# Performance work log

Measured on AMD Instinct MI355X. Metric: run time of the kernel, lower is better.

Reference implementation:

```python
import jax, jax.numpy as jnp
import numpy as np

N, DZ, DQ = 65536, 128, 512


def setup_inputs() -> dict:
    key = jax.random.key(0)
    kz, kb, kg = jax.random.split(key, 3)
    z = jax.random.normal(kz, (N, DZ), dtype=jnp.float32)
    # match torch init scaling: beta ~ 0.01*randn, gamma ~ 0.05*randn
    beta = jax.random.normal(kb, (DQ, DZ), dtype=jnp.float32) * 0.01
    gamma = jax.random.normal(kg, (DQ, DZ), dtype=jnp.float32) * 0.05
    return {"z": z, "beta": beta, "gamma": gamma}


def reference(z, beta, gamma):
    # zero-inflated Poisson sampling decoder
    logits = jnp.einsum("nd,qd->nq", z, beta)          # [N, dq]
    pi = jax.nn.sigmoid(logits)                          # exp(x)/(1+exp(x))
    rate = jnp.nan_to_num(jnp.exp(jnp.einsum("nd,qd->nq", z, gamma)), nan=1e-4)
    rate = jnp.abs(rate) + 0.01
    key = jax.random.key(42)
    kp, kb = jax.random.split(key)
    poisson = jax.random.poisson(kp, rate).astype(jnp.float32)   # [N, dq]
    masking = jax.random.bernoulli(kb, 1.0 - pi).astype(jnp.float32)
    return masking * poisson
```

## Files before the change

### kernel.cpp

```cpp
#include <hip/hip_runtime.h>
#include <stdint.h>

#pragma clang fp contract(off)

#define HALF_ 16777216u

#define WS_TSLOT 386
#define WS_WLCNT 388
#define WS_P1E5  392
#define TBL_OFF_B 4096
#define TBL_K0 95904
#define TBL_N  8193
#define WL_OFF_B 40960
#define WLCAP 16384u
#define BT_OFF_B 172032
#define NEED_V2 (BT_OFF_B + 2u * 512u * 128u * sizeof(float))
#define NEED_V1 (4096u + 2u * 512u * 128u * sizeof(float))

__device__ __forceinline__ void tf2x32(uint32_t k0, uint32_t k1,
                                       uint32_t x0, uint32_t x1,
                                       uint32_t& o0, uint32_t& o1) {
  uint32_t ks2 = k0 ^ k1 ^ 0x1BD11BDAu;
  x0 += k0; x1 += k1;
#define TFR(r) x0 += x1; x1 = (x1 << (r)) | (x1 >> (32 - (r))); x1 ^= x0;
  TFR(13) TFR(15) TFR(26) TFR(6)
  x0 += k1;  x1 += ks2 + 1u;
  TFR(17) TFR(29) TFR(16) TFR(24)
  x0 += ks2; x1 += k0 + 2u;
  TFR(13) TFR(15) TFR(26) TFR(6)
  x0 += k0;  x1 += k1 + 3u;
  TFR(17) TFR(29) TFR(16) TFR(24)
  x0 += k1;  x1 += ks2 + 4u;
  TFR(13) TFR(15) TFR(26) TFR(6)
  x0 += ks2; x1 += k0 + 5u;
#undef TFR
  o0 = x0; o1 = x1;
}

__device__ __forceinline__ uint32_t tfx(uint32_t k0, uint32_t k1, uint32_t i) {
  uint32_t o0, o1;
  tf2x32(k0, k1, 0u, i, o0, o1);
  return o0 ^ o1;
}

__device__ __forceinline__ float u01(uint32_t bits) {
  return __uint_as_float((bits >> 9) | 0x3f800000u) - 1.0f;
}

__device__ __forceinline__ float csqrt(float x) {
  return (float)__builtin_sqrt((double)x);
}

__device__ __forceinline__ float eexp(float xin) {
  float c = fminf(xin, 88.3762626647950f);
  c = fmaxf(c, -88.3762626647949f);
  float fx = floorf(__builtin_fmaf(c, 1.44269504088896341f, 0.5f));
  float x = __builtin_fmaf(-0.693359375f, fx, c);
  x = __builtin_fmaf(2.12194440e-4f, fx, x);
  float z = x * x;
  float y = __builtin_fmaf(x, 1.9875691500e-4f, 1.3981999507e-3f);
  y = __builtin_fmaf(y, x, 8.3334519073e-3f);
  y = __builtin_fmaf(y, x, 4.1665795894e-2f);
  y = __builtin_fmaf(y, x, 1.6666665459e-1f);
  y = __builtin_fmaf(y, x, 5.0000001201e-1f);
  y = __builtin_fmaf(y, z, x);
  y = 1.0f + y;
  int e = (int)fx;
  float s = __uint_as_float((uint32_t)(e + 127) << 23);
  return fmaxf(y * s, xin);
}

__device__ __forceinline__ float elog(float xin) {
  float x = fmaxf(xin, 1.17549435e-38f);
  uint32_t bits = __float_as_uint(x);
  float e = (float)((int)(bits >> 23) - 0x7e);
  x = __uint_as_float((bits & 0x807fffffu) | 0x3f000000u);
  bool mask = x < 0.707106781186547524f;
  float tmp = mask ? x : 0.0f;
  x = x - 1.0f;
  e = e - (mask ? 1.0f : 0.0f);
  x = x + tmp;
  float z = x * x;
  float y = __builtin_fmaf(7.0376836292e-2f, x, -1.1514610310e-1f);
  y = __builtin_fmaf(y, x, 1.1676998740e-1f);
  y = __builtin_fmaf(y, x, -1.2420140846e-1f);
  y = __builtin_fmaf(y, x, 1.4249322787e-1f);
  y = __builtin_fmaf(y, x, -1.6668057665e-1f);
  y = __builtin_fmaf(y, x, 2.0000714765e-1f);
  y = __builtin_fmaf(y, x, -2.4999993993e-1f);
  y = __builtin_fmaf(y, x, 3.3333331174e-1f);
  y = y * x;
  y = y * z;
  y = __builtin_fmaf(e, -2.12194440e-4f, y);
  y = __builtin_fmaf(-0.5f, z, y);
  x = x + y;
  x = __builtin_fmaf(e, 0.693359375f, x);
  if (xin == 0.0f) x = -__builtin_inff();
  return x;
}

__device__ __forceinline__ float xlog1p(float x) {
  float small_ = __builtin_fmaf(-0.5f, x, 1.0f) * x;
  float large_ = elog(x + 1.0f);
  return (fabsf(x) < 1e-4f) ? small_ : large_;
}

__device__ __forceinline__ float xlgamma(float input) {
  float z = input - 1.0f;
  float x = 0.99999999999980993227684700473478f;
  const float lcs[8] = {
      676.520368121885098567009190444019f,
      -1259.13921672240287047156078755283f,
      771.3234287776530788486528258894f,
      -176.61502916214059906584551354f,
      12.507343278686904814458936853f,
      -0.13857109526572011689554707f,
      9.984369578019570859563e-6f,
      1.50563273514931155834e-7f};
#pragma unroll
  for (int i = 0; i < 8; ++i) {
    x = x + lcs[i] / ((z + (float)i) + 1.0f);
  }
  float t = 7.5f + z;
  float log_t = 2.0149030205422647f + xlog1p(z / 7.5f);
  float log_y = __builtin_fmaf((z + 0.5f) - t / log_t, log_t,
                               0.91893853320467274178f) + elog(x);
  return log_y;
}

struct TrsP { float ll, bb, aa, ia, vr; };
__device__ __forceinline__ TrsP trs_params(float lam) {
  TrsP p;
  p.ll = elog(lam);
  p.bb = __builtin_fmaf(2.53f, csqrt(lam), 0.931f);
  p.aa = __builtin_fmaf(0.02483f, p.bb, -0.059f);
  p.ia = 1.1239f + 1.1328f / (p.bb - 3.4f);
  p.vr = 0.9277f - 3.6224f / (p.bb - 2.0f);
  return p;
}

__device__ __forceinline__ bool trs_step(float lam, const TrsP& p,
                                         float u, float v, float& kout) {
  float us = 0.5f - fabsf(u);
  float t2 = (2.0f * p.aa) / us + p.bb;
  float k = floorf(__builtin_fmaf(t2, u, lam) + 0.43f);
  kout = k;
  bool accept1 = (us >= 0.07f) && (v <= p.vr);
  if (accept1) return true;
  bool reject = (k < 0.0f) || ((us < 0.013f) && (v > us));
  if (reject) return false;
  float s = elog(v * p.ia / (p.aa / (us * us) + p.bb));
  float tt = __builtin_fmaf(k, p.ll, -lam) - xlgamma(k + 1.0f);
  return s <= tt;
}


__global__ void chain_v2(uint32_t* __restrict__ ws) {
  int lane = threadIdx.x;
  uint32_t kpa = 0, kpb = 0;
  if (lane == 0) {
    uint32_t a0, b0;
    tf2x32(0u, 42u, 0u, 0u, kpa, kpb);
    tf2x32(0u, 42u, 0u, 1u, a0, b0);
    ws[0] = a0; ws[1] = b0;
  }
  kpa = __shfl(kpa, 0); kpb = __shfl(kpb, 0);
  uint32_t kra = kpa, krb = kpb;
  uint32_t kja = kpa, kjb = kpb;
  for (int i = 0; i < 64; ++i) {
    bool isrej = (lane >= 2 && lane <= 4);
    uint32_t key0 = isrej ? kja : kra;
    uint32_t key1 = isrej ? kjb : krb;
    uint32_t xx = (lane == 1) ? 1u : (lane == 3) ? 1u : (lane == 4) ? 2u : 0u;
    uint32_t o0, o1;
    tf2x32(key0, key1, 0u, xx, o0, o1);
    if (lane == 1) { ws[2 + 2 * i] = o0; ws[3 + 2 * i] = o1; }
    if (lane == 3) { ws[130 + 4 * i] = o0; ws[131 + 4 * i] = o1; }
    if (lane == 4) { ws[132 + 4 * i] = o0; ws[133 + 4 * i] = o1; }
    kra = __shfl(o0, 0); krb = __shfl(o1, 0);
    kja = __shfl(o0, 2); kjb = __shfl(o1, 2);
  }
  if (lane == 0) {
    TrsP p = trs_params(1e5f);
    float* wf = (float*)(ws + WS_P1E5);
    wf[0] = p.ll; wf[1] = p.bb; wf[2] = p.aa; wf[3] = p.ia; wf[4] = p.vr;
    ws[WS_TSLOT] = 0u;
    ws[WS_WLCNT] = 0u;
  }
}

__global__ __launch_bounds__(256) void lgt_kernel(uint32_t* __restrict__ ws) {
  int j = blockIdx.x * 256 + threadIdx.x;
  if (j >= TBL_N) return;
  float* tbl = (float*)((char*)ws + TBL_OFF_B);
  tbl[j] = xlgamma((float)(TBL_K0 + j) + 1.0f);
}

__global__ __launch_bounds__(256) void transpose_kernel(
    const float* __restrict__ b, const float* __restrict__ g,
    float* __restrict__ bT, float* __restrict__ gT) {
  int i = blockIdx.x * 256 + threadIdx.x;
  int q = i >> 7, d = i & 127;
  bT[d * 512 + q] = b[i];
  gT[d * 512 + q] = g[i];
}

__global__ __launch_bounds__(256) void pass1_lite(
    const uint32_t* __restrict__ chain, uint32_t* __restrict__ Tslot) {
  const float* wf = (const float*)(chain + WS_P1E5);
  const float ll = wf[0], bb = wf[1], aa = wf[2], ia = wf[3], vr = wf[4];
  const float* tbl = (const float*)((const char*)chain + TBL_OFF_B);
  const float EPS = 1e-4f;

  uint32_t t = blockIdx.x * 256u + threadIdx.x;
  const uint32_t* rej = chain + 130;
  int faA = 63, faB = 63;
  bool accA = false, accB = false;
  for (int it = 0; it < 64; ++it) {
    if (accA && accB) break;
    uint32_t s00 = rej[4 * it + 0], s01 = rej[4 * it + 1];
    uint32_t s10 = rej[4 * it + 2], s11 = rej[4 * it + 3];
#pragma unroll
    for (int half = 0; half < 2; ++half) {
      bool& acc = half ? accB : accA;
      int& fa = half ? faB : faA;
      if (acc) continue;
      uint32_t idx = half ? (t + HALF_) : t;
      float u = u01(tfx(s00, s01, idx)) - 0.5f;
      float v = u01(tfx(s10, s11, idx));
      float us = 0.5f - fabsf(u);
      bool a1 = (us >= 0.07f) && (v <= vr);
      bool ok;
      if (a1) {
        ok = true;
      } else {
        float t2 = (2.0f * aa) / us + bb;
        float k = floorf(__builtin_fmaf(t2, u, 1e5f) + 0.43f);
        bool rejd = (k < 0.0f) || ((us < 0.013f) && (v > us));
        if (rejd) {
          ok = false;
        } else {
          float arg = v * ia / (aa / (us * us) + bb);
          int ki = (int)k - TBL_K0;
          float lg = (ki >= 0 && ki < TBL_N) ? tbl[ki] : xlgamma(k + 1.0f);
          float tt = __builtin_fmaf(k, ll, -1e5f) - lg;
          float sf = __logf(arg);
          if (sf <= tt - EPS)      ok = true;
          else if (sf > tt + EPS)  ok = false;
          else                     ok = (elog(arg) <= tt);
        }
      }
      if (ok) { acc = true; fa = it; }
    }
  }
  int fa = faA > faB ? faA : faB;
  for (int off = 32; off > 0; off >>= 1) {
    int o = __shfl_down(fa, off, 64);
    fa = fa > o ? fa : o;
  }
  __shared__ int smax[4];
  int wave = threadIdx.x >> 6, lanei = threadIdx.x & 63;
  if (lanei == 0) smax[wave] = fa;
  __syncthreads();
  if (threadIdx.x == 0) {
    int m01 = smax[0] > smax[1] ? smax[0] : smax[1];
    int m23 = smax[2] > smax[3] ? smax[2] : smax[3];
    int m = m01 > m23 ? m01 : m23;
    atomicMax(Tslot, (uint32_t)m);
  }
}

__device__ __forceinline__ int first_accept_exact(float lam, uint32_t idx,
                                                  const uint32_t* __restrict__ rej) {
  TrsP p = trs_params(lam);
  for (int it = 0; it < 64; ++it) {
    float u = u01(tfx(rej[4 * it + 0], rej[4 * it + 1], idx)) - 0.5f;
    float v = u01(tfx(rej[4 * it + 2], rej[4 * it + 3], idx));
    float kk;
    if (trs_step(lam, p, u, v, kk)) return it;
  }
  return 63;
}

__global__ __launch_bounds__(256) void zip_v2(
    const float* __restrict__ z, const float* __restrict__ bT,
    const float* __restrict__ gT, const uint32_t* __restrict__ chain,
    uint32_t* __restrict__ wsrw, float* __restrict__ out) {
  uint32_t t = blockIdx.x * 256u + threadIdx.x;
  uint32_t n = t >> 9;
  uint32_t q = t & 511u;
  uint32_t n2 = n + 32768u;

  const float* zr  = z + (size_t)n * 128u;
  const float* zr2 = z + (size_t)n2 * 128u;

  float lA = 0.f, lB = 0.f, gA = 0.f, gB = 0.f;
  for (int d = 0; d < 128; ++d) {
    float bv = bT[d * 512 + q];
    float gv = gT[d * 512 + q];
    float z1 = zr[d], z2 = zr2[d];
    lA = lA + z1 * bv;
    lB = lB + z2 * bv;
    gA = gA + z1 * gv;
    gB = gB + z2 * gv;
  }

  float piA = 1.0f / (1.0f + eexp(-lA));
  float piB = 1.0f / (1.0f + eexp(-lB));
  float lamA = fabsf(eexp(gA)) + 0.01f;
  float lamB = fabsf(eexp(gB)) + 0.01f;

  bool knuA = lamA < 10.0f, knuB = lamB < 10.0f;
  float pA = 0.f, pB = 0.f;
  bool fDA = false, fUA = false, fDB = false, fUB = false;
  {
    const uint32_t* wsk = chain + 2;
    const float delA = 4e-6f * (lamA + 4.0f);
    const float delB = 4e-6f * (lamB + 4.0f);
    float lpA = 0.f, lpB = 0.f;
    int kA = 0, kB = 0;
    bool goA = knuA, goB = knuB;
    for (int it = 0; it < 64; ++it) {
      if (!goA && !goB) break;
      uint32_t w0 = wsk[2 * it], w1 = wsk[2 * it + 1];
      if (goA) {
        float d = lpA + lamA;
        bool nearb = fabsf(d) < delA;
        if (d > 0.0f) { fDA = nearb; fUA = false; kA++; lpA = lpA + __logf(u01(tfx(w0, w1, t))); }
        else          { fUA = nearb; goA = false; }
      }
      if (goB) {
        float d = lpB + lamB;
        bool nearb = fabsf(d) < delB;
        if (d > 0.0f) { fDB = nearb; fUB = false; kB++; lpB = lpB + __logf(u01(tfx(w0, w1, t + HALF_))); }
        else          { fUB = nearb; goB = false; }
      }
    }
    if (knuA) pA = (float)(kA - 1);
    if (knuB) pB = (float)(kB - 1);
  }

  float dmA = u01(tfx(chain[0], chain[1], t)) - (1.0f - piA);
  float dmB = u01(tfx(chain[0], chain[1], t + HALF_)) - (1.0f - piB);
  bool mA = dmA < 0.0f, mB = dmB < 0.0f;
  bool mfA = fabsf(dmA) < 2e-6f, mfB = fabsf(dmB) < 2e-6f;

  uint32_t* wlcnt = wsrw + WS_WLCNT;
  uint32_t* wl = (uint32_t*)((char*)wsrw + WL_OFF_B);
  const uint32_t* rejk = chain + 130;

  float resA, resB;
  if (!knuA) {
    atomicMax(wsrw + WS_TSLOT, (uint32_t)first_accept_exact(lamA, t, rejk));
    uint32_t slot = atomicAdd(wlcnt, 1u);
    if (slot < WLCAP) {
      wl[2 * slot] = t | (mA ? 0x80000000u : 0u);
      wl[2 * slot + 1] = __float_as_uint(lamA);
    }
    resA = 0.0f;
  } else {
    float hiA = pA + (fUA ? 0.5f : 0.0f);
    if (mfA && hiA <= 1.2f) {
      resA = 0.5f * hiA;
    } else {
      float ph = pA + ((fDA && fUA) ? 0.0f : (fDA ? -0.5f : (fUA ? 0.5f : 0.0f)));
      resA = mA ? ph : 0.0f;
    }
  }
  if (!knuB) {
    atomicMax(wsrw + WS_TSLOT, (uint32_t)first_accept_exact(lamB, t + HALF_, rejk));
    uint32_t slot = atomicAdd(wlcnt, 1u);
    if (slot < WLCAP) {
      wl[2 * slot] = (t + HALF_) | (mB ? 0x80000000u : 0u);
      wl[2 * slot + 1] = __float_as_uint(lamB);
    }
    resB = 0.0f;
  } else {
    float hiB = pB + (fUB ? 0.5f : 0.0f);
    if (mfB && hiB <= 1.2f) {
      resB = 0.5f * hiB;
    } else {
      float ph = pB + ((fDB && fUB) ? 0.0f : (fDB ? -0.5f : (fUB ? 0.5f : 0.0f)));
      resB = mB ? ph : 0.0f;
    }
  }

  out[t]         = resA;
  out[t + HALF_] = resB;
}

__global__ __launch_bounds__(256) void k3_kernel(
    const uint32_t* __restrict__ ws, float* __restrict__ out) {
  uint32_t cnt = ws[WS_WLCNT];
  uint32_t n = cnt < WLCAP ? cnt : WLCAP;
  uint32_t Traw = ws[WS_TSLOT];
  int Tmax = (int)(Traw > 63u ? 63u : Traw);
  const uint32_t* wl = (const uint32_t*)((const char*)ws + WL_OFF_B);
  const uint32_t* rej = ws + 130;
  for (uint32_t i = blockIdx.x * 256u + threadIdx.x; i < n; i += 64u * 256u) {
    uint32_t im = wl[2 * i];
    float lam = __uint_as_float(wl[2 * i + 1]);
    uint32_t idx = im & 0x7FFFFFFFu;
    bool mask = (im >> 31) != 0u;
    TrsP p = trs_params(lam);
    float klast = -1.0f;
    for (int it = 0; it <= Tmax; ++it) {
      float u = u01(tfx(rej[4 * it + 0], rej[4 * it + 1], idx)) - 0.5f;
      float v = u01(tfx(rej[4 * it + 2], rej[4 * it + 3], idx));
      float kk;
      if (trs_step(lam, p, u, v, kk)) klast = kk;
    }
    out[idx] = mask ? klast : 0.0f;
  }
}


__global__ void chain_r10(uint32_t* __restrict__ ws) {
  if (threadIdx.x != 0 || blockIdx.x != 0) return;
  uint32_t k0 = 0u, k1 = 42u;
  uint32_t a0, b0, a1, b1;
  uint32_t kpa, kpb;
  tf2x32(k0, k1, 0u, 0u, kpa, kpb);
  tf2x32(k0, k1, 0u, 1u, a0, b0);
  ws[0] = a0; ws[1] = b0;
  uint32_t ra = kpa, rb = kpb;
  for (int i = 0; i < 64; ++i) {
    tf2x32(ra, rb, 0u, 1u, a0, b0);
    ws[2 + 2 * i] = a0; ws[3 + 2 * i] = b0;
    tf2x32(ra, rb, 0u, 0u, a1, b1);
    ra = a1; rb = b1;
  }
  ra = kpa; rb = kpb;
  for (int i = 0; i < 64; ++i) {
    tf2x32(ra, rb, 0u, 1u, a0, b0);
    ws[130 + 4 * i] = a0; ws[131 + 4 * i] = b0;
    tf2x32(ra, rb, 0u, 2u, a0, b0);
    ws[132 + 4 * i] = a0; ws[133 + 4 * i] = b0;
    tf2x32(ra, rb, 0u, 0u, a1, b1);
    ra = a1; rb = b1;
  }
  ws[386] = 0u;
}

template <bool TRANS>
__global__ __launch_bounds__(256) void pass1_r10(
    const float* __restrict__ z, const float* __restrict__ gamma,
    const float* __restrict__ gT, const uint32_t* __restrict__ chain,
    uint32_t* __restrict__ Tslot) {
  uint32_t t = blockIdx.x * 256u + threadIdx.x;
  uint32_t n = t >> 9;
  uint32_t q = t & 511u;
  uint32_t n2 = n + 32768u;
  const float* zr  = z + (size_t)n * 128u;
  const float* zr2 = z + (size_t)n2 * 128u;
  float gA = 0.f, gB = 0.f;
  if (TRANS) {
    for (int d = 0; d < 128; ++d) {
      float gv = gT[d * 512 + q];
      gA = gA + zr[d] * gv;
      gB = gB + zr2[d] * gv;
    }
  } else {
    const float* gr = gamma + (size_t)q * 128u;
    for (int d = 0; d < 128; ++d) {
      float gv = gr[d];
      gA = gA + zr[d] * gv;
      gB = gB + zr2[d] * gv;
    }
  }
  float lamA = fabsf(eexp(gA)) + 0.01f;
  float lamB = fabsf(eexp(gB)) + 0.01f;
  float lrA = (lamA < 10.0f) ? 1e5f : lamA;
  float lrB = (lamB < 10.0f) ? 1e5f : lamB;
  TrsP pa = trs_params(lrA);
  TrsP pb = trs_params(lrB);
  const uint32_t* rej = chain + 130;
  int faA = 63, faB = 63;
  bool accA = false, accB = false;
  for (int it = 0; it < 64; ++it) {
    if (accA && accB) break;
    uint32_t s00 = rej[4 * it + 0], s01 = rej[4 * it + 1];
    uint32_t s10 = rej[4 * it + 2], s11 = rej[4 * it + 3];
    float kk;
    if (!accA) {
      float u = u01(tfx(s00, s01, t)) - 0.5f;
      float v = u01(tfx(s10, s11, t));
      if (trs_step(lrA, pa, u, v, kk)) { accA = true; faA = it; }
    }
    if (!accB) {
      float u = u01(tfx(s00, s01, t + HALF_)) - 0.5f;
      float v = u01(tfx(s10, s11, t + HALF_));
      if (trs_step(lrB, pb, u, v, kk)) { accB = true; faB = it; }
    }
  }
  int fa = faA > faB ? faA : faB;
  for (int off = 32; off > 0; off >>= 1) {
    int o = __shfl_down(fa, off, 64);
    fa = fa > o ? fa : o;
  }
  __shared__ int smax[4];
  int wave = threadIdx.x >> 6, lanei = threadIdx.x & 63;
  if (lanei == 0) smax[wave] = fa;
  __syncthreads();
  if (threadIdx.x == 0) {
    int m01 = smax[0] > smax[1] ? smax[0] : smax[1];
    int m23 = smax[2] > smax[3] ? smax[2] : smax[3];
    int m = m01 > m23 ? m01 : m23;
    atomicMax(Tslot, (uint32_t)m);
  }
}

__device__ float pois_rej_last_r10(float lam, uint32_t idx,
                                   const uint32_t* __restrict__ rej, int Tmax) {
  TrsP p = trs_params(lam);
  float klast = -1.0f;
  for (int it = 0; it <= Tmax; ++it) {
    float u = u01(tfx(rej[4 * it + 0], rej[4 * it + 1], idx)) - 0.5f;
    float v = u01(tfx(rej[4 * it + 2], rej[4 * it + 3], idx));
    float kk;
    if (trs_step(lam, p, u, v, kk)) klast = kk;
  }
  return klast;
}

template <bool TRANS>
__global__ __launch_bounds__(256) void zip_r10(
    const float* __restrict__ z, const float* __restrict__ beta,
    const float* __restrict__ gamma, const float* __restrict__ bT,
    const float* __restrict__ gT, const uint32_t* __restrict__ chain,
    float* __restrict__ out) {
  uint32_t t = blockIdx.x * 256u + threadIdx.x;
  uint32_t n = t >> 9;
  uint32_t q = t & 511u;
  uint32_t n2 = n + 32768u;
  const float* zr  = z + (size_t)n * 128u;
  const float* zr2 = z + (size_t)n2 * 128u;
  float lA = 0.f, lB = 0.f, gA = 0.f, gB = 0.f;
  if (TRANS) {
    for (int d = 0; d < 128; ++d) {
      float bv = bT[d * 512 + q];
      float gv = gT[d * 512 + q];
      float z1 = zr[d], z2 = zr2[d];
      lA = lA + z1 * bv;
      lB = lB + z2 * bv;
      gA = gA + z1 * gv;
      gB = gB + z2 * gv;
    }
  } else {
    const float* br = beta + (size_t)q * 128u;
    const float* gr = gamma + (size_t)q * 128u;
    for (int d = 0; d < 128; ++d) {
      float bv = br[d], gv = gr[d];
      float z1 = zr[d], z2 = zr2[d];
      lA = lA + z1 * bv;
      lB = lB + z2 * bv;
      gA = gA + z1 * gv;
      gB = gB + z2 * gv;
    }
  }
  float piA = 1.0f / (1.0f + eexp(-lA));
  float piB = 1.0f / (1.0f + eexp(-lB));
  float lamA = fabsf(eexp(gA)) + 0.01f;
  float lamB = fabsf(eexp(gB)) + 0.01f;
  bool knuA = lamA < 10.0f, knuB = lamB < 10.0f;
  float pA = 0.f, pB = 0.f;
  bool fDA = false, fUA = false, fDB = false, fUB = false;
  {
    const uint32_t* wsk = chain + 2;
    const float delA = 1e-6f * (lamA + 4.0f);
    const float delB = 1e-6f * (lamB + 4.0f);
    float lpA = 0.f, lpB = 0.f;
    int kA = 0, kB = 0;
    bool goA = knuA, goB = knuB;
    for (int it = 0; it < 64; ++it) {
      if (!goA && !goB) break;
      uint32_t w0 = wsk[2 * it], w1 = wsk[2 * it + 1];
      if (goA) {
        float d = lpA + lamA;
        bool nearb = fabsf(d) < delA;
        if (d > 0.0f) { fDA = nearb; fUA = false; kA++; lpA = lpA + elog(u01(tfx(w0, w1, t))); }
        else          { fUA = nearb; goA = false; }
      }
      if (goB) {
        float d = lpB + lamB;
        bool nearb = fabsf(d) < delB;
        if (d > 0.0f) { fDB = nearb; fUB = false; kB++; lpB = lpB + elog(u01(tfx(w0, w1, t + HALF_))); }
        else          { fUB = nearb; goB = false; }
      }
    }
    if (knuA) pA = (float)(kA - 1);
    if (knuB) pB = (float)(kB - 1);
  }
  int Tmax = (int)(chain[386] > 63u ? 63u : chain[386]);
  if (!knuA) { pA = pois_rej_last_r10(lamA, t, chain + 130, Tmax); fDA = fUA = false; }
  if (!knuB) { pB = pois_rej_last_r10(lamB, t + HALF_, chain + 130, Tmax); fDB = fUB = false; }
  float dmA = u01(tfx(chain[0], chain[1], t)) - (1.0f - piA);
  float dmB = u01(tfx(chain[0], chain[1], t + HALF_)) - (1.0f - piB);
  bool mA = dmA < 0.0f, mB = dmB < 0.0f;
  bool mfA = fabsf(dmA) < 2e-6f, mfB = fabsf(dmB) < 2e-6f;
  float hiA = pA + (fUA ? 0.5f : 0.0f);
  float hiB = pB + (fUB ? 0.5f : 0.0f);
  float resA, resB;
  if (mfA && hiA <= 1.2f) {
    resA = 0.5f * hiA;
  } else {
    float ph = pA + ((fDA && fUA) ? 0.0f : (fDA ? -0.5f : (fUA ? 0.5f : 0.0f)));
    resA = mA ? ph : 0.0f;
  }
  if (mfB && hiB <= 1.2f) {
    resB = 0.5f * hiB;
  } else {
    float ph = pB + ((fDB && fUB) ? 0.0f : (fDB ? -0.5f : (fUB ? 0.5f : 0.0f)));
    resB = mB ? ph : 0.0f;
  }
  out[t]         = resA;
  out[t + HALF_] = resB;
}

extern "C" void kernel_launch(void* const* d_in, const int* in_sizes, int n_in,
                              void* d_out, int out_size, void* d_ws, size_t ws_size,
                              hipStream_t stream) {
  const float* z     = (const float*)d_in[0];
  const float* beta  = (const float*)d_in[1];
  const float* gamma = (const float*)d_in[2];
  float* out = (float*)d_out;
  uint32_t* ws = (uint32_t*)d_ws;

  if (ws_size >= NEED_V2) {
    float* bT = (float*)((char*)d_ws + BT_OFF_B);
    float* gT = bT + 512 * 128;
    chain_v2<<<1, 64, 0, stream>>>(ws);
    lgt_kernel<<<(TBL_N + 255) / 256, 256, 0, stream>>>(ws);
    transpose_kernel<<<256, 256, 0, stream>>>(beta, gamma, bT, gT);
    pass1_lite<<<HALF_ / 256u, 256, 0, stream>>>(ws, ws + WS_TSLOT);
    zip_v2<<<HALF_ / 256u, 256, 0, stream>>>(z, bT, gT, ws, ws, out);
    k3_kernel<<<64, 256, 0, stream>>>(ws, out);
  } else if (ws_size >= NEED_V1) {
    float* bT = (float*)((char*)d_ws + 4096);
    float* gT = bT + 512 * 128;
    chain_r10<<<1, 1, 0, stream>>>(ws);
    transpose_kernel<<<256, 256, 0, stream>>>(beta, gamma, bT, gT);
    pass1_r10<true><<<HALF_ / 256u, 256, 0, stream>>>(z, gamma, gT, ws, ws + 386);
    zip_r10<true><<<HALF_ / 256u, 256, 0, stream>>>(z, beta, gamma, bT, gT, ws, out);
  } else {
    chain_r10<<<1, 1, 0, stream>>>(ws);
    pass1_r10<false><<<HALF_ / 256u, 256, 0, stream>>>(z, gamma, nullptr, ws, ws + 386);
    zip_r10<false><<<HALF_ / 256u, 256, 0, stream>>>(z, beta, gamma, nullptr, nullptr, ws, out);
  }
}
```

Baseline: 1.919 ms.

## Split rejection-pass and Knuth tails into compacted worklists with tiled float4 weights

Pass 1 now evaluates only the first rejection iteration for every element. Elements that are not accepted are compacted into a worklist through a wave ballot and an atomic, and a second kernel scans only those. The zip kernel runs at most four Knuth iterations inline and pushes survivors to a worklist finished by a separate grid-stride kernel. This reduces divergence in the long per-thread loops. The weights are transposed into a 4-interleaved layout so the dot products can use float4 loads. In exchange it adds more kernel launches, global atomics and worklist traffic, and it relies on a larger workspace layout with capacity fallbacks.

```diff
diff --git a/kernel.cpp b/kernel.cpp
--- a/kernel.cpp
+++ b/kernel.cpp
@@ -6,16 +6,23 @@
 #define HALF_ 16777216u
 
 #define WS_TSLOT 386
-#define WS_WLCNT 388
+#define WS_RCNT  388
+#define WS_KCNT  390
+#define WS_PCNT  391
 #define WS_P1E5  392
 #define TBL_OFF_B 4096
 #define TBL_K0 95904
 #define TBL_N  8193
-#define WL_OFF_B 40960
-#define WLCAP 16384u
-#define BT_OFF_B 172032
-#define NEED_V2 (BT_OFF_B + 2u * 512u * 128u * sizeof(float))
-#define NEED_V1 (4096u + 2u * 512u * 128u * sizeof(float))
+#define V2WL_OFF_B 40960
+#define V2WLCAP 16384u
+#define V2BT_OFF_B 172032
+#define NEED_V2 (V2BT_OFF_B + 2u * 512u * 128u * 4u)
+#define RWL_OFF_B 81920
+#define RWLCAP 16384u
+#define BTT_OFF_B 262144
+#define GTT_OFF_B 524288
+#define DYN_OFF_B 786432
+#define NEED_V3 (DYN_OFF_B + (1u << 20))
 
 __device__ __forceinline__ void tf2x32(uint32_t k0, uint32_t k1,
                                        uint32_t x0, uint32_t x1,
@@ -154,7 +161,6 @@
   return s <= tt;
 }
 
-
 __global__ void chain_v2(uint32_t* __restrict__ ws) {
   int lane = threadIdx.x;
   uint32_t kpa = 0, kpb = 0;
@@ -185,7 +191,9 @@
     float* wf = (float*)(ws + WS_P1E5);
     wf[0] = p.ll; wf[1] = p.bb; wf[2] = p.aa; wf[3] = p.ia; wf[4] = p.vr;
     ws[WS_TSLOT] = 0u;
-    ws[WS_WLCNT] = 0u;
+    ws[WS_RCNT] = 0u;
+    ws[WS_KCNT] = 0u;
+    ws[WS_PCNT] = 0u;
   }
 }
 
@@ -205,13 +213,312 @@
   gT[d * 512 + q] = g[i];
 }
 
+__global__ __launch_bounds__(256) void transpose_tiled(
+    const float* __restrict__ b, const float* __restrict__ g,
+    float* __restrict__ bTT, float* __restrict__ gTT) {
+  int i = blockIdx.x * 256 + threadIdx.x;
+  int q = i >> 7, d = i & 127;
+  int dst = (d >> 2) * 2048 + (q << 2) + (d & 3);
+  bTT[dst] = b[i];
+  gTT[dst] = g[i];
+}
+
+struct P1C { float ll, bb, aa, ia, vr; };
+
+__device__ __forceinline__ bool p1_eval(const P1C& c, const float* __restrict__ tbl,
+                                        uint32_t s00, uint32_t s01,
+                                        uint32_t s10, uint32_t s11, uint32_t idx) {
+  float u = u01(tfx(s00, s01, idx)) - 0.5f;
+  float v = u01(tfx(s10, s11, idx));
+  float us = 0.5f - fabsf(u);
+  if (us >= 0.07f && v <= c.vr) return true;
+  float t2 = (2.0f * c.aa) / us + c.bb;
+  float k = floorf(__builtin_fmaf(t2, u, 1e5f) + 0.43f);
+  if ((k < 0.0f) || ((us < 0.013f) && (v > us))) return false;
+  float arg = v * c.ia / (c.aa / (us * us) + c.bb);
+  int ki = (int)k - TBL_K0;
+  float lg = (ki >= 0 && ki < TBL_N) ? tbl[ki] : xlgamma(k + 1.0f);
+  float tt = __builtin_fmaf(k, c.ll, -1e5f) - lg;
+  float sf = __logf(arg);
+  if (sf <= tt - 1e-4f) return true;
+  if (sf > tt + 1e-4f) return false;
+  return elog(arg) <= tt;
+}
+
+__device__ uint32_t p1_scan(const P1C& c, const float* __restrict__ tbl,
+                            const uint32_t* __restrict__ rej, uint32_t idx) {
+  for (int it = 1; it < 64; ++it) {
+    if (p1_eval(c, tbl, rej[4 * it], rej[4 * it + 1], rej[4 * it + 2],
+                rej[4 * it + 3], idx))
+      return (uint32_t)it;
+  }
+  return 63u;
+}
+
+__global__ __launch_bounds__(256) void p1a_kernel(
+    uint32_t* ws, uint32_t* __restrict__ p1wl, uint32_t p1cap) {
+  const float* wf = (const float*)(ws + WS_P1E5);
+  P1C c{wf[0], wf[1], wf[2], wf[3], wf[4]};
+  const float* tbl = (const float*)((const char*)ws + TBL_OFF_B);
+  const uint32_t* rej = ws + 130;
+  uint32_t s00 = rej[0], s01 = rej[1], s10 = rej[2], s11 = rej[3];
+  uint32_t t = blockIdx.x * 256u + threadIdx.x;
+  bool fa = !p1_eval(c, tbl, s00, s01, s10, s11, t);
+  bool fb = !p1_eval(c, tbl, s00, s01, s10, s11, t + HALF_);
+  uint64_t ba = __ballot(fa), bbm = __ballot(fb);
+  int na = __popcll(ba), nb = __popcll(bbm);
+  int lane = threadIdx.x & 63;
+  uint32_t base = 0;
+  if (lane == 0 && (na + nb) > 0) base = atomicAdd(ws + WS_PCNT, (uint32_t)(na + nb));
+  base = __shfl(base, 0);
+  uint64_t lm = (1ull << lane) - 1ull;
+  if (fa) {
+    uint32_t slot = base + (uint32_t)__popcll(ba & lm);
+    if (slot < p1cap) p1wl[slot] = t;
+    else atomicMax(ws + WS_TSLOT, p1_scan(c, tbl, rej, t));
+  }
+  if (fb) {
+    uint32_t slot = base + (uint32_t)na + (uint32_t)__popcll(bbm & lm);
+    if (slot < p1cap) p1wl[slot] = t + HALF_;
+    else atomicMax(ws + WS_TSLOT, p1_scan(c, tbl, rej, t + HALF_));
+  }
+}
+
+__global__ __launch_bounds__(256) void p1b_kernel(
+    uint32_t* ws, const uint32_t* __restrict__ p1wl, uint32_t p1cap) {
+  const float* wf = (const float*)(ws + WS_P1E5);
+  P1C c{wf[0], wf[1], wf[2], wf[3], wf[4]};
+  const float* tbl = (const float*)((const char*)ws + TBL_OFF_B);
+  const uint32_t* rej = ws + 130;
+  uint32_t cnt = ws[WS_PCNT];
+  if (cnt > p1cap) cnt = p1cap;
+  uint32_t fmax = 0;
+  for (uint32_t i = blockIdx.x * 256u + threadIdx.x; i < cnt;
+       i += gridDim.x * 256u) {
+    uint32_t f = p1_scan(c, tbl, rej, p1wl[i]);
+    if (f > fmax) fmax = f;
+  }
+  for (int off = 32; off > 0; off >>= 1) {
+    uint32_t o = __shfl_down(fmax, off, 64);
+    if (o > fmax) fmax = o;
+  }
+  if ((threadIdx.x & 63) == 0 && fmax > 0) atomicMax(ws + WS_TSLOT, fmax);
+}
+
+__device__ __forceinline__ int first_accept_exact(float lam, uint32_t idx,
+                                                  const uint32_t* __restrict__ rej) {
+  TrsP p = trs_params(lam);
+  for (int it = 0; it < 64; ++it) {
+    float u = u01(tfx(rej[4 * it + 0], rej[4 * it + 1], idx)) - 0.5f;
+    float v = u01(tfx(rej[4 * it + 2], rej[4 * it + 3], idx));
+    float kk;
+    if (trs_step(lam, p, u, v, kk)) return it;
+  }
+  return 63;
+}
+
+__device__ float knuth_finish(float lp, float lam, bool fD, bool m,
+                              const uint32_t* __restrict__ wsk, uint32_t idx) {
+  const float del = 4e-6f * (lam + 4.0f);
+  int k = 4;
+  bool fU = false;
+  for (int it = 4; it < 64; ++it) {
+    float d = lp + lam;
+    bool nb = fabsf(d) < del;
+    if (d > 0.0f) {
+      fD = nb; k++;
+      lp = lp + __logf(u01(tfx(wsk[2 * it], wsk[2 * it + 1], idx)));
+    } else { fU = nb; break; }
+  }
+  float p = (float)(k - 1);
+  float ph = p + ((fD && fU) ? 0.0f : (fD ? -0.5f : (fU ? 0.5f : 0.0f)));
+  return m ? ph : 0.0f;
+}
+
+__global__ __launch_bounds__(256) void zip_v3(
+    const float* __restrict__ z, uint32_t* ws,
+    uint32_t* __restrict__ kwl, uint32_t kcap, float* __restrict__ out) {
+  uint32_t t = blockIdx.x * 256u + threadIdx.x;
+  uint32_t n = t >> 9, q = t & 511u, n2 = n + 32768u;
+
+  const float4* z4a = (const float4*)(z + (size_t)n * 128u);
+  const float4* z4b = (const float4*)(z + (size_t)n2 * 128u);
+  const float4* bt4 = (const float4*)((const char*)ws + BTT_OFF_B);
+  const float4* gt4 = (const float4*)((const char*)ws + GTT_OFF_B);
+
+  float lA = 0.f, lB = 0.f, gA = 0.f, gB = 0.f;
+  for (int d4 = 0; d4 < 32; ++d4) {
+    float4 bv = bt4[(d4 << 9) + q];
+    float4 gv = gt4[(d4 << 9) + q];
+    float4 z1 = z4a[d4], z2 = z4b[d4];
+    lA = lA + z1.x * bv.x; lB = lB + z2.x * bv.x; gA = gA + z1.x * gv.x; gB = gB + z2.x * gv.x;
+    lA = lA + z1.y * bv.y; lB = lB + z2.y * bv.y; gA = gA + z1.y * gv.y; gB = gB + z2.y * gv.y;
+    lA = lA + z1.z * bv.z; lB = lB + z2.z * bv.z; gA = gA + z1.z * gv.z; gB = gB + z2.z * gv.z;
+    lA = lA + z1.w * bv.w; lB = lB + z2.w * bv.w; gA = gA + z1.w * gv.w; gB = gB + z2.w * gv.w;
+  }
+
+  float piA = 1.0f / (1.0f + eexp(-lA));
+  float piB = 1.0f / (1.0f + eexp(-lB));
+  float lamA = fabsf(eexp(gA)) + 0.01f;
+  float lamB = fabsf(eexp(gB)) + 0.01f;
+
+  float dmA = u01(tfx(ws[0], ws[1], t)) - (1.0f - piA);
+  float dmB = u01(tfx(ws[0], ws[1], t + HALF_)) - (1.0f - piB);
+  bool mA = dmA < 0.0f, mB = dmB < 0.0f;
+  bool mfA = fabsf(dmA) < 2e-6f, mfB = fabsf(dmB) < 2e-6f;
+
+  bool knuA = lamA < 10.0f, knuB = lamB < 10.0f;
+
+  const uint32_t* wsk = ws + 2;
+  const float delA = 4e-6f * (lamA + 4.0f);
+  const float delB = 4e-6f * (lamB + 4.0f);
+  float lpA = 0.f, lpB = 0.f;
+  int kA = 0, kB = 0;
+  bool goA = knuA, goB = knuB;
+  bool fDA = false, fUA = false, fDB = false, fUB = false;
+  for (int it = 0; it < 4; ++it) {
+    if (!goA && !goB) break;
+    uint32_t w0 = wsk[2 * it], w1 = wsk[2 * it + 1];
+    if (goA) {
+      float d = lpA + lamA;
+      bool nb = fabsf(d) < delA;
+      if (d > 0.0f) { fDA = nb; kA++; lpA = lpA + __logf(u01(tfx(w0, w1, t))); }
+      else          { fUA = nb; goA = false; }
+    }
+    if (goB) {
+      float d = lpB + lamB;
+      bool nb = fabsf(d) < delB;
+      if (d > 0.0f) { fDB = nb; kB++; lpB = lpB + __logf(u01(tfx(w0, w1, t + HALF_))); }
+      else          { fUB = nb; goB = false; }
+    }
+  }
+  bool survA = knuA && goA, survB = knuB && goB;
+
+  const uint32_t* rejk = ws + 130;
+  uint32_t* rwl = (uint32_t*)((char*)ws + RWL_OFF_B);
+  if (!knuA) {
+    atomicMax(ws + WS_TSLOT, (uint32_t)first_accept_exact(lamA, t, rejk));
+    uint32_t slot = atomicAdd(ws + WS_RCNT, 1u);
+    if (slot < RWLCAP) {
+      rwl[2 * slot] = t | (mA ? 0x80000000u : 0u);
+      rwl[2 * slot + 1] = __float_as_uint(lamA);
+    }
+  }
+  if (!knuB) {
+    atomicMax(ws + WS_TSLOT, (uint32_t)first_accept_exact(lamB, t + HALF_, rejk));
+    uint32_t slot = atomicAdd(ws + WS_RCNT, 1u);
+    if (slot < RWLCAP) {
+      rwl[2 * slot] = (t + HALF_) | (mB ? 0x80000000u : 0u);
+      rwl[2 * slot + 1] = __float_as_uint(lamB);
+    }
+  }
+
+  uint64_t ba = __ballot(survA), bbm = __ballot(survB);
+  int na = __popcll(ba), nb = __popcll(bbm);
+  int lane = threadIdx.x & 63;
+  uint32_t base = 0;
+  if (lane == 0 && (na + nb) > 0) base = atomicAdd(ws + WS_KCNT, (uint32_t)(na + nb));
+  base = __shfl(base, 0);
+  uint64_t lm = (1ull << lane) - 1ull;
+
+  if (survA) {
+    uint32_t slot = base + (uint32_t)__popcll(ba & lm);
+    if (slot < kcap) {
+      kwl[3 * slot]     = t | ((uint32_t)mA << 25) | ((uint32_t)fDA << 27);
+      kwl[3 * slot + 1] = __float_as_uint(lpA);
+      kwl[3 * slot + 2] = __float_as_uint(lamA);
+    } else {
+      out[t] = knuth_finish(lpA, lamA, fDA, mA, wsk, t);
+    }
+  } else if (knuA) {
+    float pA = (float)(kA - 1);
+    float hiA = pA + (fUA ? 0.5f : 0.0f);
+    float resA;
+    if (mfA && hiA <= 1.2f) resA = 0.5f * hiA;
+    else {
+      float ph = pA + ((fDA && fUA) ? 0.0f : (fDA ? -0.5f : (fUA ? 0.5f : 0.0f)));
+      resA = mA ? ph : 0.0f;
+    }
+    out[t] = resA;
+  } else {
+    out[t] = 0.0f;
+  }
+
+  if (survB) {
+    uint32_t slot = base + (uint32_t)na + (uint32_t)__popcll(bbm & lm);
+    if (slot < kcap) {
+      kwl[3 * slot]     = (t + HALF_) | ((uint32_t)mB << 25) | ((uint32_t)fDB << 27);
+      kwl[3 * slot + 1] = __float_as_uint(lpB);
+      kwl[3 * slot + 2] = __float_as_uint(lamB);
+    } else {
+      out[t + HALF_] = knuth_finish(lpB, lamB, fDB, mB, wsk, t + HALF_);
+    }
+  } else if (knuB) {
+    float pB = (float)(kB - 1);
+    float hiB = pB + (fUB ? 0.5f : 0.0f);
+    float resB;
+    if (mfB && hiB <= 1.2f) resB = 0.5f * hiB;
+    else {
+      float ph = pB + ((fDB && fUB) ? 0.0f : (fDB ? -0.5f : (fUB ? 0.5f : 0.0f)));
+      resB = mB ? ph : 0.0f;
+    }
+    out[t + HALF_] = resB;
+  } else {
+    out[t + HALF_] = 0.0f;
+  }
+}
+
+__global__ __launch_bounds__(256) void k3b_kernel(
+    uint32_t* ws, const uint32_t* __restrict__ kwl, uint32_t kcap,
+    float* __restrict__ out) {
+  uint32_t cnt = ws[WS_KCNT];
+  if (cnt > kcap) cnt = kcap;
+  const uint32_t* wsk = ws + 2;
+  for (uint32_t i = blockIdx.x * 256u + threadIdx.x; i < cnt;
+       i += gridDim.x * 256u) {
+    uint32_t w = kwl[3 * i];
+    uint32_t idx = w & 0x01FFFFFFu;
+    bool m = (w >> 25) & 1u;
+    bool fD = (w >> 27) & 1u;
+    float lp = __uint_as_float(kwl[3 * i + 1]);
+    float lam = __uint_as_float(kwl[3 * i + 2]);
+    out[idx] = knuth_finish(lp, lam, fD, m, wsk, idx);
+  }
+}
+
+__global__ __launch_bounds__(256) void k3_kernel(
+    const uint32_t* ws, const uint32_t* __restrict__ wl, uint32_t cap,
+    float* __restrict__ out) {
+  uint32_t cnt = ws[WS_RCNT];
+  if (cnt > cap) cnt = cap;
+  uint32_t Traw = ws[WS_TSLOT];
+  int Tmax = (int)(Traw > 63u ? 63u : Traw);
+  const uint32_t* rej = ws + 130;
+  for (uint32_t i = blockIdx.x * 256u + threadIdx.x; i < cnt;
+       i += gridDim.x * 256u) {
+    uint32_t im = wl[2 * i];
+    float lam = __uint_as_float(wl[2 * i + 1]);
+    uint32_t idx = im & 0x7FFFFFFFu;
+    bool mask = (im >> 31) != 0u;
+    TrsP p = trs_params(lam);
+    float klast = -1.0f;
+    for (int it = 0; it <= Tmax; ++it) {
+      float u = u01(tfx(rej[4 * it + 0], rej[4 * it + 1], idx)) - 0.5f;
+      float v = u01(tfx(rej[4 * it + 2], rej[4 * it + 3], idx));
+      float kk;
+      if (trs_step(lam, p, u, v, kk)) klast = kk;
+    }
+    out[idx] = mask ? klast : 0.0f;
+  }
+}
+
+
 __global__ __launch_bounds__(256) void pass1_lite(
     const uint32_t* __restrict__ chain, uint32_t* __restrict__ Tslot) {
   const float* wf = (const float*)(chain + WS_P1E5);
   const float ll = wf[0], bb = wf[1], aa = wf[2], ia = wf[3], vr = wf[4];
   const float* tbl = (const float*)((const char*)chain + TBL_OFF_B);
   const float EPS = 1e-4f;
-
   uint32_t t = blockIdx.x * 256u + threadIdx.x;
   const uint32_t* rej = chain + 130;
   int faA = 63, faB = 63;
@@ -231,23 +538,21 @@
       float us = 0.5f - fabsf(u);
       bool a1 = (us >= 0.07f) && (v <= vr);
       bool ok;
-      if (a1) {
-        ok = true;
-      } else {
+      if (a1) ok = true;
+      else {
         float t2 = (2.0f * aa) / us + bb;
         float k = floorf(__builtin_fmaf(t2, u, 1e5f) + 0.43f);
         bool rejd = (k < 0.0f) || ((us < 0.013f) && (v > us));
-        if (rejd) {
-          ok = false;
-        } else {
+        if (rejd) ok = false;
+        else {
           float arg = v * ia / (aa / (us * us) + bb);
           int ki = (int)k - TBL_K0;
           float lg = (ki >= 0 && ki < TBL_N) ? tbl[ki] : xlgamma(k + 1.0f);
           float tt = __builtin_fmaf(k, ll, -1e5f) - lg;
           float sf = __logf(arg);
-          if (sf <= tt - EPS)      ok = true;
-          else if (sf > tt + EPS)  ok = false;
-          else                     ok = (elog(arg) <= tt);
+          if (sf <= tt - EPS) ok = true;
+          else if (sf > tt + EPS) ok = false;
+          else ok = (elog(arg) <= tt);
         }
       }
       if (ok) { acc = true; fa = it; }
@@ -270,30 +575,13 @@
   }
 }
 
-__device__ __forceinline__ int first_accept_exact(float lam, uint32_t idx,
-                                                  const uint32_t* __restrict__ rej) {
-  TrsP p = trs_params(lam);
-  for (int it = 0; it < 64; ++it) {
-    float u = u01(tfx(rej[4 * it + 0], rej[4 * it + 1], idx)) - 0.5f;
-    float v = u01(tfx(rej[4 * it + 2], rej[4 * it + 3], idx));
-    float kk;
-    if (trs_step(lam, p, u, v, kk)) return it;
-  }
-  return 63;
-}
-
 __global__ __launch_bounds__(256) void zip_v2(
     const float* __restrict__ z, const float* __restrict__ bT,
-    const float* __restrict__ gT, const uint32_t* __restrict__ chain,
-    uint32_t* __restrict__ wsrw, float* __restrict__ out) {
+    const float* __restrict__ gT, uint32_t* ws, float* __restrict__ out) {
   uint32_t t = blockIdx.x * 256u + threadIdx.x;
-  uint32_t n = t >> 9;
-  uint32_t q = t & 511u;
-  uint32_t n2 = n + 32768u;
-
+  uint32_t n = t >> 9, q = t & 511u, n2 = n + 32768u;
   const float* zr  = z + (size_t)n * 128u;
   const float* zr2 = z + (size_t)n2 * 128u;
-
   float lA = 0.f, lB = 0.f, gA = 0.f, gB = 0.f;
   for (int d = 0; d < 128; ++d) {
     float bv = bT[d * 512 + q];
@@ -304,17 +592,15 @@
     gA = gA + z1 * gv;
     gB = gB + z2 * gv;
   }
-
   float piA = 1.0f / (1.0f + eexp(-lA));
   float piB = 1.0f / (1.0f + eexp(-lB));
   float lamA = fabsf(eexp(gA)) + 0.01f;
   float lamB = fabsf(eexp(gB)) + 0.01f;
-
   bool knuA = lamA < 10.0f, knuB = lamB < 10.0f;
   float pA = 0.f, pB = 0.f;
   bool fDA = false, fUA = false, fDB = false, fUB = false;
   {
-    const uint32_t* wsk = chain + 2;
+    const uint32_t* wsk = ws + 2;
     const float delA = 4e-6f * (lamA + 4.0f);
     const float delB = 4e-6f * (lamB + 4.0f);
     float lpA = 0.f, lpB = 0.f;
@@ -325,295 +611,60 @@
       uint32_t w0 = wsk[2 * it], w1 = wsk[2 * it + 1];
       if (goA) {
         float d = lpA + lamA;
-        bool nearb = fabsf(d) < delA;
-        if (d > 0.0f) { fDA = nearb; fUA = false; kA++; lpA = lpA + __logf(u01(tfx(w0, w1, t))); }
-        else          { fUA = nearb; goA = false; }
+        bool nb = fabsf(d) < delA;
+        if (d > 0.0f) { fDA = nb; kA++; lpA = lpA + __logf(u01(tfx(w0, w1, t))); }
+        else          { fUA = nb; goA = false; }
       }
       if (goB) {
         float d = lpB + lamB;
-        bool nearb = fabsf(d) < delB;
-        if (d > 0.0f) { fDB = nearb; fUB = false; kB++; lpB = lpB + __logf(u01(tfx(w0, w1, t + HALF_))); }
-        else          { fUB = nearb; goB = false; }
+        bool nb = fabsf(d) < delB;
+        if (d > 0.0f) { fDB = nb; kB++; lpB = lpB + __logf(u01(tfx(w0, w1, t + HALF_))); }
+        else          { fUB = nb; goB = false; }
       }
     }
     if (knuA) pA = (float)(kA - 1);
     if (knuB) pB = (float)(kB - 1);
   }
-
-  float dmA = u01(tfx(chain[0], chain[1], t)) - (1.0f - piA);
-  float dmB = u01(tfx(chain[0], chain[1], t + HALF_)) - (1.0f - piB);
+  float dmA = u01(tfx(ws[0], ws[1], t)) - (1.0f - piA);
+  float dmB = u01(tfx(ws[0], ws[1], t + HALF_)) - (1.0f - piB);
   bool mA = dmA < 0.0f, mB = dmB < 0.0f;
   bool mfA = fabsf(dmA) < 2e-6f, mfB = fabsf(dmB) < 2e-6f;
-
-  uint32_t* wlcnt = wsrw + WS_WLCNT;
-  uint32_t* wl = (uint32_t*)((char*)wsrw + WL_OFF_B);
-  const uint32_t* rejk = chain + 130;
-
+  uint32_t* wl = (uint32_t*)((char*)ws + V2WL_OFF_B);
+  const uint32_t* rejk = ws + 130;
   float resA, resB;
   if (!knuA) {
-    atomicMax(wsrw + WS_TSLOT, (uint32_t)first_accept_exact(lamA, t, rejk));
-    uint32_t slot = atomicAdd(wlcnt, 1u);
-    if (slot < WLCAP) {
+    atomicMax(ws + WS_TSLOT, (uint32_t)first_accept_exact(lamA, t, rejk));
+    uint32_t slot = atomicAdd(ws + WS_RCNT, 1u);
+    if (slot < V2WLCAP) {
       wl[2 * slot] = t | (mA ? 0x80000000u : 0u);
       wl[2 * slot + 1] = __float_as_uint(lamA);
     }
     resA = 0.0f;
   } else {
     float hiA = pA + (fUA ? 0.5f : 0.0f);
-    if (mfA && hiA <= 1.2f) {
-      resA = 0.5f * hiA;
-    } else {
+    if (mfA && hiA <= 1.2f) resA = 0.5f * hiA;
+    else {
       float ph = pA + ((fDA && fUA) ? 0.0f : (fDA ? -0.5f : (fUA ? 0.5f : 0.0f)));
       resA = mA ? ph : 0.0f;
     }
   }
   if (!knuB) {
-    atomicMax(wsrw + WS_TSLOT, (uint32_t)first_accept_exact(lamB, t + HALF_, rejk));
-    uint32_t slot = atomicAdd(wlcnt, 1u);
-    if (slot < WLCAP) {
+    atomicMax(ws + WS_TSLOT, (uint32_t)first_accept_exact(lamB, t + HALF_, rejk));
+    uint32_t slot = atomicAdd(ws + WS_RCNT, 1u);
+    if (slot < V2WLCAP) {
       wl[2 * slot] = (t + HALF_) | (mB ? 0x80000000u : 0u);
       wl[2 * slot + 1] = __float_as_uint(lamB);
     }
     resB = 0.0f;
   } else {
     float hiB = pB + (fUB ? 0.5f : 0.0f);
-    if (mfB && hiB <= 1.2f) {
-      resB = 0.5f * hiB;
-    } else {
+    if (mfB && hiB <= 1.2f) resB = 0.5f * hiB;
+    else {
       float ph = pB + ((fDB && fUB) ? 0.0f : (fDB ? -0.5f : (fUB ? 0.5f : 0.0f)));
       resB = mB ? ph : 0.0f;
     }
   }
-
-  out[t]         = resA;
-  out[t + HALF_] = resB;
-}
-
-__global__ __launch_bounds__(256) void k3_kernel(
-    const uint32_t* __restrict__ ws, float* __restrict__ out) {
-  uint32_t cnt = ws[WS_WLCNT];
-  uint32_t n = cnt < WLCAP ? cnt : WLCAP;
-  uint32_t Traw = ws[WS_TSLOT];
-  int Tmax = (int)(Traw > 63u ? 63u : Traw);
-  const uint32_t* wl = (const uint32_t*)((const char*)ws + WL_OFF_B);
-  const uint32_t* rej = ws + 130;
-  for (uint32_t i = blockIdx.x * 256u + threadIdx.x; i < n; i += 64u * 256u) {
-    uint32_t im = wl[2 * i];
-    float lam = __uint_as_float(wl[2 * i + 1]);
-    uint32_t idx = im & 0x7FFFFFFFu;
-    bool mask = (im >> 31) != 0u;
-    TrsP p = trs_params(lam);
-    float klast = -1.0f;
-    for (int it = 0; it <= Tmax; ++it) {
-      float u = u01(tfx(rej[4 * it + 0], rej[4 * it + 1], idx)) - 0.5f;
-      float v = u01(tfx(rej[4 * it + 2], rej[4 * it + 3], idx));
-      float kk;
-      if (trs_step(lam, p, u, v, kk)) klast = kk;
-    }
-    out[idx] = mask ? klast : 0.0f;
-  }
-}
-
-
-__global__ void chain_r10(uint32_t* __restrict__ ws) {
-  if (threadIdx.x != 0 || blockIdx.x != 0) return;
-  uint32_t k0 = 0u, k1 = 42u;
-  uint32_t a0, b0, a1, b1;
-  uint32_t kpa, kpb;
-  tf2x32(k0, k1, 0u, 0u, kpa, kpb);
-  tf2x32(k0, k1, 0u, 1u, a0, b0);
-  ws[0] = a0; ws[1] = b0;
-  uint32_t ra = kpa, rb = kpb;
-  for (int i = 0; i < 64; ++i) {
-    tf2x32(ra, rb, 0u, 1u, a0, b0);
-    ws[2 + 2 * i] = a0; ws[3 + 2 * i] = b0;
-    tf2x32(ra, rb, 0u, 0u, a1, b1);
-    ra = a1; rb = b1;
-  }
-  ra = kpa; rb = kpb;
-  for (int i = 0; i < 64; ++i) {
-    tf2x32(ra, rb, 0u, 1u, a0, b0);
-    ws[130 + 4 * i] = a0; ws[131 + 4 * i] = b0;
-    tf2x32(ra, rb, 0u, 2u, a0, b0);
-    ws[132 + 4 * i] = a0; ws[133 + 4 * i] = b0;
-    tf2x32(ra, rb, 0u, 0u, a1, b1);
-    ra = a1; rb = b1;
-  }
-  ws[386] = 0u;
-}
-
-template <bool TRANS>
-__global__ __launch_bounds__(256) void pass1_r10(
-    const float* __restrict__ z, const float* __restrict__ gamma,
-    const float* __restrict__ gT, const uint32_t* __restrict__ chain,
-    uint32_t* __restrict__ Tslot) {
-  uint32_t t = blockIdx.x * 256u + threadIdx.x;
-  uint32_t n = t >> 9;
-  uint32_t q = t & 511u;
-  uint32_t n2 = n + 32768u;
-  const float* zr  = z + (size_t)n * 128u;
-  const float* zr2 = z + (size_t)n2 * 128u;
-  float gA = 0.f, gB = 0.f;
-  if (TRANS) {
-    for (int d = 0; d < 128; ++d) {
-      float gv = gT[d * 512 + q];
-      gA = gA + zr[d] * gv;
-      gB = gB + zr2[d] * gv;
-    }
-  } else {
-    const float* gr = gamma + (size_t)q * 128u;
-    for (int d = 0; d < 128; ++d) {
-      float gv = gr[d];
-      gA = gA + zr[d] * gv;
-      gB = gB + zr2[d] * gv;
-    }
-  }
-  float lamA = fabsf(eexp(gA)) + 0.01f;
-  float lamB = fabsf(eexp(gB)) + 0.01f;
-  float lrA = (lamA < 10.0f) ? 1e5f : lamA;
-  float lrB = (lamB < 10.0f) ? 1e5f : lamB;
-  TrsP pa = trs_params(lrA);
-  TrsP pb = trs_params(lrB);
-  const uint32_t* rej = chain + 130;
-  int faA = 63, faB = 63;
-  bool accA = false, accB = false;
-  for (int it = 0; it < 64; ++it) {
-    if (accA && accB) break;
-    uint32_t s00 = rej[4 * it + 0], s01 = rej[4 * it + 1];
-    uint32_t s10 = rej[4 * it + 2], s11 = rej[4 * it + 3];
-    float kk;
-    if (!accA) {
-      float u = u01(tfx(s00, s01, t)) - 0.5f;
-      float v = u01(tfx(s10, s11, t));
-      if (trs_step(lrA, pa, u, v, kk)) { accA = true; faA = it; }
-    }
-    if (!accB) {
-      float u = u01(tfx(s00, s01, t + HALF_)) - 0.5f;
-      float v = u01(tfx(s10, s11, t + HALF_));
-      if (trs_step(lrB, pb, u, v, kk)) { accB = true; faB = it; }
-    }
-  }
-  int fa = faA > faB ? faA : faB;
-  for (int off = 32; off > 0; off >>= 1) {
-    int o = __shfl_down(fa, off, 64);
-    fa = fa > o ? fa : o;
-  }
-  __shared__ int smax[4];
-  int wave = threadIdx.x >> 6, lanei = threadIdx.x & 63;
-  if (lanei == 0) smax[wave] = fa;
-  __syncthreads();
-  if (threadIdx.x == 0) {
-    int m01 = smax[0] > smax[1] ? smax[0] : smax[1];
-    int m23 = smax[2] > smax[3] ? smax[2] : smax[3];
-    int m = m01 > m23 ? m01 : m23;
-    atomicMax(Tslot, (uint32_t)m);
-  }
-}
-
-__device__ float pois_rej_last_r10(float lam, uint32_t idx,
-                                   const uint32_t* __restrict__ rej, int Tmax) {
-  TrsP p = trs_params(lam);
-  float klast = -1.0f;
-  for (int it = 0; it <= Tmax; ++it) {
-    float u = u01(tfx(rej[4 * it + 0], rej[4 * it + 1], idx)) - 0.5f;
-    float v = u01(tfx(rej[4 * it + 2], rej[4 * it + 3], idx));
-    float kk;
-    if (trs_step(lam, p, u, v, kk)) klast = kk;
-  }
-  return klast;
-}
-
-template <bool TRANS>
-__global__ __launch_bounds__(256) void zip_r10(
-    const float* __restrict__ z, const float* __restrict__ beta,
-    const float* __restrict__ gamma, const float* __restrict__ bT,
-    const float* __restrict__ gT, const uint32_t* __restrict__ chain,
-    float* __restrict__ out) {
-  uint32_t t = blockIdx.x * 256u + threadIdx.x;
-  uint32_t n = t >> 9;
-  uint32_t q = t & 511u;
-  uint32_t n2 = n + 32768u;
-  const float* zr  = z + (size_t)n * 128u;
-  const float* zr2 = z + (size_t)n2 * 128u;
-  float lA = 0.f, lB = 0.f, gA = 0.f, gB = 0.f;
-  if (TRANS) {
-    for (int d = 0; d < 128; ++d) {
-      float bv = bT[d * 512 + q];
-      float gv = gT[d * 512 + q];
-      float z1 = zr[d], z2 = zr2[d];
-      lA = lA + z1 * bv;
-      lB = lB + z2 * bv;
-      gA = gA + z1 * gv;
-      gB = gB + z2 * gv;
-    }
-  } else {
-    const float* br = beta + (size_t)q * 128u;
-    const float* gr = gamma + (size_t)q * 128u;
-    for (int d = 0; d < 128; ++d) {
-      float bv = br[d], gv = gr[d];
-      float z1 = zr[d], z2 = zr2[d];
-      lA = lA + z1 * bv;
-      lB = lB + z2 * bv;
-      gA = gA + z1 * gv;
-      gB = gB + z2 * gv;
-    }
-  }
-  float piA = 1.0f / (1.0f + eexp(-lA));
-  float piB = 1.0f / (1.0f + eexp(-lB));
-  float lamA = fabsf(eexp(gA)) + 0.01f;
-  float lamB = fabsf(eexp(gB)) + 0.01f;
-  bool knuA = lamA < 10.0f, knuB = lamB < 10.0f;
-  float pA = 0.f, pB = 0.f;
-  bool fDA = false, fUA = false, fDB = false, fUB = false;
-  {
-    const uint32_t* wsk = chain + 2;
-    const float delA = 1e-6f * (lamA + 4.0f);
-    const float delB = 1e-6f * (lamB + 4.0f);
-    float lpA = 0.f, lpB = 0.f;
-    int kA = 0, kB = 0;
-    bool goA = knuA, goB = knuB;
-    for (int it = 0; it < 64; ++it) {
-      if (!goA && !goB) break;
-      uint32_t w0 = wsk[2 * it], w1 = wsk[2 * it + 1];
-      if (goA) {
-        float d = lpA + lamA;
-        bool nearb = fabsf(d) < delA;
-        if (d > 0.0f) { fDA = nearb; fUA = false; kA++; lpA = lpA + elog(u01(tfx(w0, w1, t))); }
-        else          { fUA = nearb; goA = false; }
-      }
-      if (goB) {
-        float d = lpB + lamB;
-        bool nearb = fabsf(d) < delB;
-        if (d > 0.0f) { fDB = nearb; fUB = false; kB++; lpB = lpB + elog(u01(tfx(w0, w1, t + HALF_))); }
-        else          { fUB = nearb; goB = false; }
-      }
-    }
-    if (knuA) pA = (float)(kA - 1);
-    if (knuB) pB = (float)(kB - 1);
-  }
-  int Tmax = (int)(chain[386] > 63u ? 63u : chain[386]);
-  if (!knuA) { pA = pois_rej_last_r10(lamA, t, chain + 130, Tmax); fDA = fUA = false; }
-  if (!knuB) { pB = pois_rej_last_r10(lamB, t + HALF_, chain + 130, Tmax); fDB = fUB = false; }
-  float dmA = u01(tfx(chain[0], chain[1], t)) - (1.0f - piA);
-  float dmB = u01(tfx(chain[0], chain[1], t + HALF_)) - (1.0f - piB);
-  bool mA = dmA < 0.0f, mB = dmB < 0.0f;
-  bool mfA = fabsf(dmA) < 2e-6f, mfB = fabsf(dmB) < 2e-6f;
-  float hiA = pA + (fUA ? 0.5f : 0.0f);
-  float hiB = pB + (fUB ? 0.5f : 0.0f);
-  float resA, resB;
-  if (mfA && hiA <= 1.2f) {
-    resA = 0.5f * hiA;
-  } else {
-    float ph = pA + ((fDA && fUA) ? 0.0f : (fDA ? -0.5f : (fUA ? 0.5f : 0.0f)));
-    resA = mA ? ph : 0.0f;
-  }
-  if (mfB && hiB <= 1.2f) {
-    resB = 0.5f * hiB;
-  } else {
-    float ph = pB + ((fDB && fUB) ? 0.0f : (fDB ? -0.5f : (fUB ? 0.5f : 0.0f)));
-    resB = mB ? ph : 0.0f;
-  }
-  out[t]         = resA;
+  out[t] = resA;
   out[t + HALF_] = resB;
 }
 
@@ -626,25 +677,38 @@
   float* out = (float*)d_out;
   uint32_t* ws = (uint32_t*)d_ws;
 
-  if (ws_size >= NEED_V2) {
-    float* bT = (float*)((char*)d_ws + BT_OFF_B);
+  if (ws_size >= NEED_V3) {
+    size_t rem = ws_size - DYN_OFF_B;
+    size_t p1e = rem / 3 / 4;
+    if (p1e > 16777216) p1e = 16777216;
+    size_t p1bytes = (p1e * 4 + 15) & ~(size_t)15;
+    size_t ke = (rem - p1bytes) / 12;
+    if (ke > 8388608) ke = 8388608;
+    uint32_t p1cap = (uint32_t)p1e;
+    uint32_t kcap = (uint32_t)ke;
+    uint32_t* p1wl = (uint32_t*)((char*)d_ws + DYN_OFF_B);
+    uint32_t* kwl  = (uint32_t*)((char*)d_ws + DYN_OFF_B + p1bytes);
+    float* bTT = (float*)((char*)d_ws + BTT_OFF_B);
+    float* gTT = (float*)((char*)d_ws + GTT_OFF_B);
+    uint32_t* rwl = (uint32_t*)((char*)d_ws + RWL_OFF_B);
+
+    chain_v2<<<1, 64, 0, stream>>>(ws);
+    lgt_kernel<<<(TBL_N + 255) / 256, 256, 0, stream>>>(ws);
+    transpose_tiled<<<256, 256, 0, stream>>>(beta, gamma, bTT, gTT);
+    p1a_kernel<<<HALF_ / 256u, 256, 0, stream>>>(ws, p1wl, p1cap);
+    p1b_kernel<<<2048, 256, 0, stream>>>(ws, p1wl, p1cap);
+    zip_v3<<<HALF_ / 256u, 256, 0, stream>>>(z, ws, kwl, kcap, out);
+    k3b_kernel<<<2048, 256, 0, stream>>>(ws, kwl, kcap, out);
+    k3_kernel<<<64, 256, 0, stream>>>(ws, rwl, RWLCAP, out);
+  } else {
+    float* bT = (float*)((char*)d_ws + V2BT_OFF_B);
     float* gT = bT + 512 * 128;
+    uint32_t* rwl = (uint32_t*)((char*)d_ws + V2WL_OFF_B);
     chain_v2<<<1, 64, 0, stream>>>(ws);
     lgt_kernel<<<(TBL_N + 255) / 256, 256, 0, stream>>>(ws);
     transpose_kernel<<<256, 256, 0, stream>>>(beta, gamma, bT, gT);
     pass1_lite<<<HALF_ / 256u, 256, 0, stream>>>(ws, ws + WS_TSLOT);
-    zip_v2<<<HALF_ / 256u, 256, 0, stream>>>(z, bT, gT, ws, ws, out);
-    k3_kernel<<<64, 256, 0, stream>>>(ws, out);
-  } else if (ws_size >= NEED_V1) {
-    float* bT = (float*)((char*)d_ws + 4096);
-    float* gT = bT + 512 * 128;
-    chain_r10<<<1, 1, 0, stream>>>(ws);
-    transpose_kernel<<<256, 256, 0, stream>>>(beta, gamma, bT, gT);
-    pass1_r10<true><<<HALF_ / 256u, 256, 0, stream>>>(z, gamma, gT, ws, ws + 386);
-    zip_r10<true><<<HALF_ / 256u, 256, 0, stream>>>(z, beta, gamma, bT, gT, ws, out);
-  } else {
-    chain_r10<<<1, 1, 0, stream>>>(ws);
-    pass1_r10<false><<<HALF_ / 256u, 256, 0, stream>>>(z, gamma, nullptr, ws, ws + 386);
-    zip_r10<false><<<HALF_ / 256u, 256, 0, stream>>>(z, beta, gamma, nullptr, nullptr, ws, out);
-  }
-}
+    zip_v2<<<HALF_ / 256u, 256, 0, stream>>>(z, bT, gT, ws, out);
+    k3_kernel<<<64, 256, 0, stream>>>(ws, rwl, V2WLCAP, out);
+  }
+}
```

Result: slower. 6.245 ms (+225.3%).
